# Kernel tuning notes

Hardware: AMD Instinct MI355X
Metric: run time of the kernel (lower is better)

The kernel has to match this reference:

```python
import jax, jax.numpy as jnp
import numpy as np

NUM_HEADS = 8
NEG_MASK = -1000.0  # original code masks with -1000, not -inf


def setup_inputs() -> dict:
    key = jax.random.key(0)
    ks = jax.random.split(key, 12)
    B, S, D = 4, 2048, 512
    HID, OUT = 512, 512
    dh = D // NUM_HEADS      # 64, per-head input dim
    eh = HID // NUM_HEADS    # 64, per-head hidden dim
    w = 0.02
    return {
        "q": jax.random.normal(ks[0], (B, S, D), dtype=jnp.float32),
        "k": jax.random.normal(ks[1], (B, S, D), dtype=jnp.float32),
        "v": jax.random.normal(ks[2], (B, S, D), dtype=jnp.float32),
        # Linear weights stored as [in, out] (transpose of torch convention)
        "Wq": jax.random.normal(ks[3], (dh, eh), dtype=jnp.float32) * w,
        "bq": jax.random.normal(ks[4], (eh,), dtype=jnp.float32) * w,
        "Wk": jax.random.normal(ks[5], (dh, eh), dtype=jnp.float32) * w,
        "bk": jax.random.normal(ks[6], (eh,), dtype=jnp.float32) * w,
        "Wv": jax.random.normal(ks[7], (dh, eh), dtype=jnp.float32) * w,
        "bv": jax.random.normal(ks[8], (eh,), dtype=jnp.float32) * w,
        "Wo": jax.random.normal(ks[9], (HID, OUT), dtype=jnp.float32) * w,
        "bo": jax.random.normal(ks[10], (OUT,), dtype=jnp.float32) * w,
        "valid_lens": jnp.maximum(jax.random.randint(ks[11], (B,), 0, S), 1),
        "max_len": S,
    }


def reference(q, k, v, Wq, bq, Wk, bk, Wv, bv, Wo, bo, valid_lens, max_len):
    B, S, D = q.shape
    H = NUM_HEADS
    # split into heads: [B, S, H, dh]; note the SAME projection weights are
    # shared across heads (as in the original module)
    qh = q.reshape(B, S, H, D // H)
    kh = k.reshape(B, S, H, D // H)
    vh = v.reshape(B, S, H, D // H)
    qp = jnp.einsum('bshd,de->bshe', qh, Wq) + bq  # [B,S,H,eh]
    kp = jnp.einsum('bshd,de->bshe', kh, Wk) + bk
    vp = jnp.einsum('bshd,de->bshe', vh, Wv) + bv
    scale = 1.0 / jnp.sqrt(jnp.asarray(qp.shape[-1], qp.dtype))
    scores = jnp.einsum('bshe,bthe->bhst', qp, kp) * scale  # [B,H,S,S]
    # key-padding mask: positions j >= valid_len get -1000 (original semantics)
    key_mask = jnp.arange(S)[None, :] < valid_lens[:, None]  # [B,S]
    scores = jnp.where(key_mask[:, None, None, :], scores, NEG_MASK)
    attn = jax.nn.softmax(scores, axis=-1)
    ctx = jnp.einsum('bhst,bthe->bshe', attn, vp).reshape(B, S, -1)  # head-major concat
    return jnp.einsum('bse,eo->bso', ctx, Wo) + bo
```

## Files before the change

### kernel.cpp

```cpp
#include <hip/hip_runtime.h>

#define S_LEN 2048
#define D_MODEL 512

typedef __attribute__((ext_vector_type(8))) short s8v;
typedef __attribute__((ext_vector_type(4))) float f4v;
typedef __attribute__((ext_vector_type(4))) short s4v;
typedef __attribute__((ext_vector_type(4))) int   i4v;
typedef __attribute__((ext_vector_type(2))) int   i2v;

#define MFMA __builtin_amdgcn_mfma_f32_16x16x32_bf16

__device__ inline short f2bf(float x) {
    union { float f; unsigned u; } v; v.f = x;
    unsigned r = v.u + 0x7fffu + ((v.u >> 16) & 1u);
    return (short)(r >> 16);
}
__device__ inline unsigned pack_bf2_trunc(float a, float b) {
    unsigned ua = __builtin_bit_cast(unsigned, a);
    unsigned ub = __builtin_bit_cast(unsigned, b);
    return (ua >> 16) | (ub & 0xffff0000u);
}

template <int C>
__device__ inline float dppf(float x) {
    int i = __builtin_bit_cast(int, x);
    i = __builtin_amdgcn_update_dpp(0, i, C, 0xF, 0xF, true);
    return __builtin_bit_cast(float, i);
}
__device__ inline float rowsum16(float x) {
    x += dppf<0xB1>(x);
    x += dppf<0x4E>(x);
    x += dppf<0x141>(x);
    x += dppf<0x140>(x);
    return x;
}

typedef const __attribute__((address_space(1))) void* gptr_t;
typedef __attribute__((address_space(3))) void* sptr_t;
__device__ inline void gload16(const void* g, void* s) {
    __builtin_amdgcn_global_load_lds((gptr_t)g, (sptr_t)s, 16, 0, 0);
}

__global__ __launch_bounds__(256) void prep_kernel(
    const float* __restrict__ Wo, short* __restrict__ WoT)
{
    __shared__ short t[64 * 65];
    const int bi = (blockIdx.x >> 3) * 64;
    const int bj = (blockIdx.x & 7) * 64;
    const int c = threadIdx.x & 63, rr = threadIdx.x >> 6;
#pragma unroll
    for (int r = 0; r < 16; r++) {
        int i = r * 4 + rr;
        t[c * 65 + i] = f2bf(Wo[(size_t)(bi + i) * 512 + bj + c]);
    }
    __syncthreads();
#pragma unroll
    for (int r = 0; r < 16; r++) {
        int o = r * 4 + rr;
        WoT[(size_t)(bj + o) * 512 + bi + c] = t[o * 65 + c];
    }
}

__global__ __launch_bounds__(256) void proj_kernel(
    const float* __restrict__ q, const float* __restrict__ k, const float* __restrict__ v,
    const float* __restrict__ Wq, const float* __restrict__ Wk, const float* __restrict__ Wv,
    const float* __restrict__ bq, const float* __restrict__ bk, const float* __restrict__ bv,
    short* __restrict__ qp, short* __restrict__ kfrag, short* __restrict__ vfrag)
{
    __shared__ short sm[128 * 64];

    const int t = blockIdx.z >> 2;
    const int b = blockIdx.z & 3;
    const int h = blockIdx.y;
    const int qt = blockIdx.x;
    const int w = threadIdx.x >> 6, lane = threadIdx.x & 63;
    const int l = lane & 15, qd = lane >> 4;

    const float* X    = (t == 0) ? q  : (t == 1) ? k  : v;
    const float* Wp   = (t == 0) ? Wq : (t == 1) ? Wk : Wv;
    const float* bias = (t == 0) ? bq : (t == 1) ? bk : bv;

    {
        const int d = threadIdx.x >> 2, c4 = threadIdx.x & 3;
        const float* src = Wp + d * 64 + c4 * 16;
        f4v x0 = *(const f4v*)(src);
        f4v x1 = *(const f4v*)(src + 4);
        f4v x2 = *(const f4v*)(src + 8);
        f4v x3 = *(const f4v*)(src + 12);
        float xs[16] = {x0[0],x0[1],x0[2],x0[3], x1[0],x1[1],x1[2],x1[3],
                        x2[0],x2[1],x2[2],x2[3], x3[0],x3[1],x3[2],x3[3]};
#pragma unroll
        for (int j = 0; j < 16; j++) {
            int e = c4 * 16 + j;
            int sidx = (e * 64 + d) ^ (((e >> 2) & 7) << 3);
            sm[sidx] = f2bf(xs[j]);
        }
    }
    __syncthreads();

    const int s0 = qt * 128 + w * 32;

    s8v a[2][2];
#pragma unroll
    for (int mt = 0; mt < 2; mt++)
#pragma unroll
        for (int kk = 0; kk < 2; kk++) {
            const float* p = X + (size_t)(b * S_LEN + s0 + mt * 16 + l) * 512 + h * 64 + kk * 32 + qd * 8;
            f4v x0 = *(const f4v*)p;
            f4v x1 = *(const f4v*)(p + 4);
            s8v fr;
            fr[0] = f2bf(x0[0]); fr[1] = f2bf(x0[1]); fr[2] = f2bf(x0[2]); fr[3] = f2bf(x0[3]);
            fr[4] = f2bf(x1[0]); fr[5] = f2bf(x1[1]); fr[6] = f2bf(x1[2]); fr[7] = f2bf(x1[3]);
            a[mt][kk] = fr;
        }
    s8v wf[4][2];
#pragma unroll
    for (int nt = 0; nt < 4; nt++) {
        int wrow = (t < 2) ? (4 * l + nt) : (nt * 16 + l);
        int key = ((wrow >> 2) & 7) << 3;
#pragma unroll
        for (int kk = 0; kk < 2; kk++)
            wf[nt][kk] = *(const s8v*)(sm + ((wrow * 64 + kk * 32 + qd * 8) ^ key));
    }

    const f4v fz = {0.f, 0.f, 0.f, 0.f};
    f4v acc[2][4];
#pragma unroll
    for (int mt = 0; mt < 2; mt++)
#pragma unroll
        for (int nt = 0; nt < 4; nt++) acc[mt][nt] = fz;

#pragma unroll
    for (int kk = 0; kk < 2; kk++)
#pragma unroll
        for (int nt = 0; nt < 4; nt++)
#pragma unroll
            for (int mt = 0; mt < 2; mt++)
                acc[mt][nt] = MFMA(a[mt][kk], wf[nt][kk], acc[mt][nt], 0, 0, 0);

    const float SC = 0.125f * 1.442695041f;

    if (t == 0) {
        float bbs[4];
#pragma unroll
        for (int nt = 0; nt < 4; nt++) bbs[nt] = bias[4 * l + nt];
#pragma unroll
        for (int mt = 0; mt < 2; mt++)
#pragma unroll
            for (int r = 0; r < 4; r++) {
                int s = s0 + mt * 16 + qd * 4 + r;
                s4v pk;
#pragma unroll
                for (int nt = 0; nt < 4; nt++)
                    pk[nt] = f2bf((acc[mt][nt][r] + bbs[nt]) * SC);
                *(s4v*)(qp + ((size_t)(b * 8 + h) * S_LEN + s) * 64 + 4 * l) = pk;
            }
        return;
    }

    __syncthreads();

    if (t == 1) {
        float bbs[4];
#pragma unroll
        for (int nt = 0; nt < 4; nt++) bbs[nt] = bias[4 * l + nt];
#pragma unroll
        for (int mt = 0; mt < 2; mt++)
#pragma unroll
            for (int r = 0; r < 4; r++) {
                int sl = w * 32 + mt * 16 + qd * 4 + r;
                s4v pk;
#pragma unroll
                for (int nt = 0; nt < 4; nt++) pk[nt] = f2bf(acc[mt][nt][r] + bbs[nt]);
                int sidx = (sl * 64 + 4 * l) ^ (((sl >> 2) & 7) << 3);
                *(s4v*)(sm + sidx) = pk;
            }
    } else {
#pragma unroll
        for (int nt = 0; nt < 4; nt++) {
            float bb = bias[nt * 16 + l];
            int e = nt * 16 + l;
            int key = ((e >> 2) & 7) << 3;
#pragma unroll
            for (int mt = 0; mt < 2; mt++) {
                s4v pk;
#pragma unroll
                for (int r = 0; r < 4; r++) pk[r] = f2bf(acc[mt][nt][r] + bb);
                int sidx = (e * 128 + w * 32 + mt * 16 + qd * 4) ^ key;
                *(s4v*)(sm + sidx) = pk;
            }
        }
    }
    __syncthreads();

    short* dst = (t == 1) ? kfrag : vfrag;
    const size_t obase0 = ((size_t)(b * 8 + h) * 32 + qt * 2) * 4096;
    const int f = threadIdx.x & 63, cp = threadIdx.x >> 6;
    const int fl = f & 15, fq = f >> 4;
#pragma unroll
    for (int tt = 0; tt < 2; tt++)
#pragma unroll
        for (int ci = 0; ci < 2; ci++) {
            int c = cp + ci * 4;
            int n2 = c >> 1, kk = c & 1;
            int sidx;
            if (t == 1) {
                int sl = tt * 64 + 4 * fl + n2;
                sidx = (sl * 64 + kk * 32 + fq * 8) ^ (((sl >> 2) & 7) << 3);
            } else {
                int e = 4 * fl + n2;
                sidx = (e * 128 + tt * 64 + kk * 32 + fq * 8) ^ (((e >> 2) & 7) << 3);
            }
            s8v x = *(const s8v*)(sm + sidx);
            *(s8v*)(dst + obase0 + tt * 4096 + c * 512 + f * 8) = x;
        }
}

__global__ __launch_bounds__(256, 2) void attn_kernel(
    const short* __restrict__ qp, const short* __restrict__ kfrag,
    const short* __restrict__ vfrag,
    const int* __restrict__ valid_lens, short* __restrict__ ctx)
{
    __shared__ alignas(16) short kbuf[2][8192];
    __shared__ alignas(16) short lP[4][32 * 72];

    const int gid = blockIdx.x;
    const int h  = gid & 7;
    int b        = (gid >> 3) & 3;
    const int qt = gid >> 5;
    b ^= 3 * ((gid >> 8) & 1);
    const int w = threadIdx.x >> 6, lane = threadIdx.x & 63;
    const int l = lane & 15, qd = lane >> 4;
    const int vlen = valid_lens[b];
    const int nt2 = (vlen + 127) >> 7;

    const int bh = b * 8 + h;
    const short* Qs = qp + (size_t)bh * S_LEN * 64;
    const short* Kf = kfrag + (size_t)bh * 32 * 4096;
    const short* Vf = vfrag + (size_t)bh * 32 * 4096;

    const int s0 = qt * 128 + w * 32;
    s8v qf[2][2];
#pragma unroll
    for (int mt = 0; mt < 2; mt++)
#pragma unroll
        for (int kk = 0; kk < 2; kk++)
            qf[mt][kk] = *(const s8v*)(Qs + (size_t)(s0 + mt * 16 + l) * 64 + kk * 32 + qd * 8);

    const f4v fz = {0.f, 0.f, 0.f, 0.f};
    f4v O[2][4];
    float lsum[2][4];
#pragma unroll
    for (int mt = 0; mt < 2; mt++)
#pragma unroll
        for (int r = 0; r < 4; r++) lsum[mt][r] = 0.f;
#pragma unroll
    for (int mt = 0; mt < 2; mt++)
#pragma unroll
        for (int ne = 0; ne < 4; ne++) O[mt][ne] = fz;

    short* lPw = lP[w];
    const int toff = threadIdx.x * 8;

#pragma unroll
    for (int r = 0; r < 4; r++)
        gload16(Kf + r * 2048 + toff, &kbuf[0][r * 2048 + toff]);
    __syncthreads();

    for (int j = 0; j < nt2; j++) {
        const int cur = j & 1;
        if (j + 1 < nt2) {
            const short* Ks = Kf + (size_t)(j + 1) * 8192;
#pragma unroll
            for (int r = 0; r < 4; r++)
                gload16(Ks + r * 2048 + toff, &kbuf[cur ^ 1][r * 2048 + toff]);
        }

#pragma unroll
        for (int st = 0; st < 2; st++) {
            const int kb = 2 * j + st;

            const short* Vb = Vf + (size_t)kb * 4096 + lane * 8;
            s8v vf[4][2];
#pragma unroll
            for (int ne = 0; ne < 4; ne++)
#pragma unroll
                for (int kk = 0; kk < 2; kk++)
                    vf[ne][kk] = *(const s8v*)(Vb + (ne * 2 + kk) * 512);

            const short* Kb = &kbuf[cur][st * 4096 + lane * 8];
            s8v kf[4][2];
#pragma unroll
            for (int nt = 0; nt < 4; nt++)
#pragma unroll
                for (int kk = 0; kk < 2; kk++)
                    kf[nt][kk] = *(const s8v*)(Kb + (nt * 2 + kk) * 512);

            f4v sf[2][4];
#pragma unroll
            for (int mt = 0; mt < 2; mt++)
#pragma unroll
                for (int nt = 0; nt < 4; nt++) sf[mt][nt] = fz;
            __builtin_amdgcn_s_setprio(1);
#pragma unroll
            for (int nt = 0; nt < 4; nt++)
#pragma unroll
                for (int mt = 0; mt < 2; mt++) {
                    sf[mt][nt] = MFMA(qf[mt][0], kf[nt][0], sf[mt][nt], 0, 0, 0);
                    sf[mt][nt] = MFMA(qf[mt][1], kf[nt][1], sf[mt][nt], 0, 0, 0);
                }
            __builtin_amdgcn_s_setprio(0);

            if (j == nt2 - 1) {
                int rem = vlen - kb * 64;
                if (rem < 64) {
#pragma unroll
                    for (int nt = 0; nt < 4; nt++)
                        if (4 * l + nt >= rem) {
#pragma unroll
                            for (int mt = 0; mt < 2; mt++)
#pragma unroll
                                for (int r = 0; r < 4; r++) sf[mt][nt][r] = -1e30f;
                        }
                }
            }

#pragma unroll
            for (int mt = 0; mt < 2; mt++)
#pragma unroll
                for (int r = 0; r < 4; r++) {
                    float p0 = __builtin_amdgcn_exp2f(sf[mt][0][r]);
                    float p1 = __builtin_amdgcn_exp2f(sf[mt][1][r]);
                    float p2 = __builtin_amdgcn_exp2f(sf[mt][2][r]);
                    float p3 = __builtin_amdgcn_exp2f(sf[mt][3][r]);
                    lsum[mt][r] += (p0 + p1) + (p2 + p3);
                    i2v pk;
                    pk[0] = (int)pack_bf2_trunc(p0, p1);
                    pk[1] = (int)pack_bf2_trunc(p2, p3);
                    *(i2v*)(lPw + (mt * 16 + qd * 4 + r) * 72 + 4 * l) = pk;
                }

            s8v pa[2][2];
#pragma unroll
            for (int mt = 0; mt < 2; mt++)
#pragma unroll
                for (int kk = 0; kk < 2; kk++)
                    pa[mt][kk] = *(const s8v*)(lPw + (mt * 16 + l) * 72 + kk * 32 + qd * 8);
            __builtin_amdgcn_s_setprio(1);
#pragma unroll
            for (int ne = 0; ne < 4; ne++)
#pragma unroll
                for (int mt = 0; mt < 2; mt++) {
                    O[mt][ne] = MFMA(pa[mt][0], vf[ne][0], O[mt][ne], 0, 0, 0);
                    O[mt][ne] = MFMA(pa[mt][1], vf[ne][1], O[mt][ne], 0, 0, 0);
                }
            __builtin_amdgcn_s_setprio(0);
        }

        __syncthreads();
    }

#pragma unroll
    for (int mt = 0; mt < 2; mt++)
#pragma unroll
        for (int r = 0; r < 4; r++) {
            float inv = 1.0f / rowsum16(lsum[mt][r]);
            int s = s0 + mt * 16 + qd * 4 + r;
            s4v pk;
#pragma unroll
            for (int ne = 0; ne < 4; ne++) pk[ne] = f2bf(O[mt][ne][r] * inv);
            *(s4v*)(ctx + ((size_t)(b * S_LEN + s)) * 512 + h * 64 + 4 * l) = pk;
        }
}

__global__ __launch_bounds__(256) void outproj_kernel(
    const short* __restrict__ ctx, const short* __restrict__ WoT,
    const float* __restrict__ bo, float* __restrict__ out)
{
    __shared__ short lB[64 * 520];

    const int rb = blockIdx.x * 128;
    const int nb = blockIdx.y * 64;
    const int w = threadIdx.x >> 6, lane = threadIdx.x & 63;
    const int l = lane & 15, qd = lane >> 4;

    {
        int n = threadIdx.x >> 2, c0 = threadIdx.x & 3;
#pragma unroll
        for (int i = 0; i < 16; i++) {
            int g = i * 4 + c0;
            i4v x = *(const i4v*)(WoT + (size_t)(nb + n) * 512 + g * 8);
            *(i4v*)(lB + n * 520 + g * 8) = x;
        }
    }
    __syncthreads();

    const f4v fz = {0.f, 0.f, 0.f, 0.f};
    f4v acc[2][4];
#pragma unroll
    for (int mt = 0; mt < 2; mt++)
#pragma unroll
        for (int nt = 0; nt < 4; nt++) acc[mt][nt] = fz;

    const short* actx0 = ctx + (size_t)(rb + w * 32 + l) * 512 + qd * 8;
    const short* actx1 = actx0 + (size_t)16 * 512;

    s8v afA[2], afB[2];
    afA[0] = *(const s8v*)(actx0);
    afA[1] = *(const s8v*)(actx1);

#pragma unroll
    for (int ko = 0; ko < 16; ko += 2) {
        afB[0] = *(const s8v*)(actx0 + (ko + 1) * 32);
        afB[1] = *(const s8v*)(actx1 + (ko + 1) * 32);
#pragma unroll
        for (int nt = 0; nt < 4; nt++) {
            s8v bfr = *(const s8v*)(lB + (nt * 16 + l) * 520 + ko * 32 + qd * 8);
#pragma unroll
            for (int mt = 0; mt < 2; mt++)
                acc[mt][nt] = MFMA(afA[mt], bfr, acc[mt][nt], 0, 0, 0);
        }
        if (ko + 2 < 16) {
            afA[0] = *(const s8v*)(actx0 + (ko + 2) * 32);
            afA[1] = *(const s8v*)(actx1 + (ko + 2) * 32);
        }
#pragma unroll
        for (int nt = 0; nt < 4; nt++) {
            s8v bfr = *(const s8v*)(lB + (nt * 16 + l) * 520 + (ko + 1) * 32 + qd * 8);
#pragma unroll
            for (int mt = 0; mt < 2; mt++)
                acc[mt][nt] = MFMA(afB[mt], bfr, acc[mt][nt], 0, 0, 0);
        }
    }

#pragma unroll
    for (int nt = 0; nt < 4; nt++) {
        float bias = bo[nb + nt * 16 + l];
#pragma unroll
        for (int mt = 0; mt < 2; mt++)
#pragma unroll
            for (int r = 0; r < 4; r++) {
                int row = rb + w * 32 + mt * 16 + qd * 4 + r;
                out[(size_t)row * 512 + nb + nt * 16 + l] = acc[mt][nt][r] + bias;
            }
    }
}

extern "C" void kernel_launch(void* const* d_in, const int* in_sizes, int n_in,
                              void* d_out, int out_size, void* d_ws, size_t ws_size,
                              hipStream_t stream)
{
    const float* q  = (const float*)d_in[0];
    const float* k  = (const float*)d_in[1];
    const float* v  = (const float*)d_in[2];
    const float* Wq = (const float*)d_in[3];
    const float* bq = (const float*)d_in[4];
    const float* Wk = (const float*)d_in[5];
    const float* bk = (const float*)d_in[6];
    const float* Wv = (const float*)d_in[7];
    const float* bv = (const float*)d_in[8];
    const float* Wo = (const float*)d_in[9];
    const float* bo = (const float*)d_in[10];
    const int*   vl = (const int*)d_in[11];
    float* out = (float*)d_out;

    char* ws = (char*)d_ws;
    const size_t SL = (size_t)4 * 8 * S_LEN * 64 * sizeof(short);
    short* qp    = (short*)(ws);
    short* ctx   = (short*)(ws + SL);
    short* kfrag = (short*)(ws + 2 * SL);
    short* vfrag = (short*)(ws + 3 * SL);
    short* WoT   = (short*)(ws + 4 * SL);

    prep_kernel<<<64, 256, 0, stream>>>(Wo, WoT);
    proj_kernel<<<dim3(16, 8, 12), 256, 0, stream>>>(q, k, v, Wq, Wk, Wv,
                                                     bq, bk, bv, qp, kfrag, vfrag);
    attn_kernel<<<512, 256, 0, stream>>>(qp, kfrag, vfrag, vl, ctx);
    outproj_kernel<<<dim3(64, 8), 256, 0, stream>>>(ctx, WoT, bo, out);
}
```

Baseline: 166.2 us.

## Fuse Q projection into attention kernel prologue

Moves the Q projection out of the separate projection kernel and into the start of the attention kernel. Each attention block now loads its fp32 query rows, projects them with MFMA against Wq staged in shared memory, and passes the scaled bf16 result through shared memory into registers. This removes the qp intermediate write and read-back in global memory and one third of the projection grid. In exchange it adds extra syncs and prologue latency in the attention kernel, and reuses kbuf and lP shared buffers as scratch.

```diff
diff --git a/kernel.cpp b/kernel.cpp
--- a/kernel.cpp
+++ b/kernel.cpp
@@ -63,23 +63,23 @@
 }
 
 __global__ __launch_bounds__(256) void proj_kernel(
-    const float* __restrict__ q, const float* __restrict__ k, const float* __restrict__ v,
-    const float* __restrict__ Wq, const float* __restrict__ Wk, const float* __restrict__ Wv,
-    const float* __restrict__ bq, const float* __restrict__ bk, const float* __restrict__ bv,
-    short* __restrict__ qp, short* __restrict__ kfrag, short* __restrict__ vfrag)
+    const float* __restrict__ k, const float* __restrict__ v,
+    const float* __restrict__ Wk, const float* __restrict__ Wv,
+    const float* __restrict__ bk, const float* __restrict__ bv,
+    short* __restrict__ kfrag, short* __restrict__ vfrag)
 {
     __shared__ short sm[128 * 64];
 
-    const int t = blockIdx.z >> 2;
+    const int t2 = blockIdx.z >> 2;
     const int b = blockIdx.z & 3;
     const int h = blockIdx.y;
     const int qt = blockIdx.x;
     const int w = threadIdx.x >> 6, lane = threadIdx.x & 63;
     const int l = lane & 15, qd = lane >> 4;
 
-    const float* X    = (t == 0) ? q  : (t == 1) ? k  : v;
-    const float* Wp   = (t == 0) ? Wq : (t == 1) ? Wk : Wv;
-    const float* bias = (t == 0) ? bq : (t == 1) ? bk : bv;
+    const float* X    = (t2 == 0) ? k  : v;
+    const float* Wp   = (t2 == 0) ? Wk : Wv;
+    const float* bias = (t2 == 0) ? bk : bv;
 
     {
         const int d = threadIdx.x >> 2, c4 = threadIdx.x & 3;
@@ -117,7 +117,7 @@
     s8v wf[4][2];
 #pragma unroll
     for (int nt = 0; nt < 4; nt++) {
-        int wrow = (t < 2) ? (4 * l + nt) : (nt * 16 + l);
+        int wrow = (t2 == 0) ? (4 * l + nt) : (nt * 16 + l);
         int key = ((wrow >> 2) & 7) << 3;
 #pragma unroll
         for (int kk = 0; kk < 2; kk++)
@@ -139,29 +139,9 @@
             for (int mt = 0; mt < 2; mt++)
                 acc[mt][nt] = MFMA(a[mt][kk], wf[nt][kk], acc[mt][nt], 0, 0, 0);
 
-    const float SC = 0.125f * 1.442695041f;
-
-    if (t == 0) {
-        float bbs[4];
-#pragma unroll
-        for (int nt = 0; nt < 4; nt++) bbs[nt] = bias[4 * l + nt];
-#pragma unroll
-        for (int mt = 0; mt < 2; mt++)
-#pragma unroll
-            for (int r = 0; r < 4; r++) {
-                int s = s0 + mt * 16 + qd * 4 + r;
-                s4v pk;
-#pragma unroll
-                for (int nt = 0; nt < 4; nt++)
-                    pk[nt] = f2bf((acc[mt][nt][r] + bbs[nt]) * SC);
-                *(s4v*)(qp + ((size_t)(b * 8 + h) * S_LEN + s) * 64 + 4 * l) = pk;
-            }
-        return;
-    }
-
-    __syncthreads();
-
-    if (t == 1) {
+    __syncthreads();
+
+    if (t2 == 0) {
         float bbs[4];
 #pragma unroll
         for (int nt = 0; nt < 4; nt++) bbs[nt] = bias[4 * l + nt];
@@ -194,7 +174,7 @@
     }
     __syncthreads();
 
-    short* dst = (t == 1) ? kfrag : vfrag;
+    short* dst = (t2 == 0) ? kfrag : vfrag;
     const size_t obase0 = ((size_t)(b * 8 + h) * 32 + qt * 2) * 4096;
     const int f = threadIdx.x & 63, cp = threadIdx.x >> 6;
     const int fl = f & 15, fq = f >> 4;
@@ -205,7 +185,7 @@
             int c = cp + ci * 4;
             int n2 = c >> 1, kk = c & 1;
             int sidx;
-            if (t == 1) {
+            if (t2 == 0) {
                 int sl = tt * 64 + 4 * fl + n2;
                 sidx = (sl * 64 + kk * 32 + fq * 8) ^ (((sl >> 2) & 7) << 3);
             } else {
@@ -218,8 +198,8 @@
 }
 
 __global__ __launch_bounds__(256, 2) void attn_kernel(
-    const short* __restrict__ qp, const short* __restrict__ kfrag,
-    const short* __restrict__ vfrag,
+    const float* __restrict__ q, const float* __restrict__ Wq, const float* __restrict__ bq,
+    const short* __restrict__ kfrag, const short* __restrict__ vfrag,
     const int* __restrict__ valid_lens, short* __restrict__ ctx)
 {
     __shared__ alignas(16) short kbuf[2][8192];
@@ -236,19 +216,105 @@
     const int nt2 = (vlen + 127) >> 7;
 
     const int bh = b * 8 + h;
-    const short* Qs = qp + (size_t)bh * S_LEN * 64;
     const short* Kf = kfrag + (size_t)bh * 32 * 4096;
     const short* Vf = vfrag + (size_t)bh * 32 * 4096;
 
     const int s0 = qt * 128 + w * 32;
+    const f4v fz = {0.f, 0.f, 0.f, 0.f};
+    const float SC = 0.125f * 1.442695041f;
+
+    short* lPw = lP[w];
+    const int toff = threadIdx.x * 8;
+
+#pragma unroll
+    for (int r = 0; r < 4; r++)
+        gload16(Kf + r * 2048 + toff, &kbuf[0][r * 2048 + toff]);
+
+    short* wsm = &kbuf[1][0];
+    short* qsm = &lP[0][0];
+    {
+        const int d = threadIdx.x >> 2, c4 = threadIdx.x & 3;
+        const float* src = Wq + d * 64 + c4 * 16;
+        f4v x0 = *(const f4v*)(src);
+        f4v x1 = *(const f4v*)(src + 4);
+        f4v x2 = *(const f4v*)(src + 8);
+        f4v x3 = *(const f4v*)(src + 12);
+        float xs[16] = {x0[0],x0[1],x0[2],x0[3], x1[0],x1[1],x1[2],x1[3],
+                        x2[0],x2[1],x2[2],x2[3], x3[0],x3[1],x3[2],x3[3]};
+#pragma unroll
+        for (int j = 0; j < 16; j++) {
+            int e = c4 * 16 + j;
+            int sidx = (e * 64 + d) ^ (((e >> 2) & 7) << 3);
+            wsm[sidx] = f2bf(xs[j]);
+        }
+    }
+    __syncthreads();
+
+    {
+        s8v a[2][2];
+#pragma unroll
+        for (int mt = 0; mt < 2; mt++)
+#pragma unroll
+            for (int kk = 0; kk < 2; kk++) {
+                const float* p = q + (size_t)(b * S_LEN + s0 + mt * 16 + l) * 512 + h * 64 + kk * 32 + qd * 8;
+                f4v x0 = *(const f4v*)p;
+                f4v x1 = *(const f4v*)(p + 4);
+                s8v fr;
+                fr[0] = f2bf(x0[0]); fr[1] = f2bf(x0[1]); fr[2] = f2bf(x0[2]); fr[3] = f2bf(x0[3]);
+                fr[4] = f2bf(x1[0]); fr[5] = f2bf(x1[1]); fr[6] = f2bf(x1[2]); fr[7] = f2bf(x1[3]);
+                a[mt][kk] = fr;
+            }
+        s8v wf2[4][2];
+#pragma unroll
+        for (int nt = 0; nt < 4; nt++) {
+            int wrow = 4 * l + nt;
+            int key = ((wrow >> 2) & 7) << 3;
+#pragma unroll
+            for (int kk = 0; kk < 2; kk++)
+                wf2[nt][kk] = *(const s8v*)(wsm + ((wrow * 64 + kk * 32 + qd * 8) ^ key));
+        }
+        f4v qacc[2][4];
+#pragma unroll
+        for (int mt = 0; mt < 2; mt++)
+#pragma unroll
+            for (int nt = 0; nt < 4; nt++) qacc[mt][nt] = fz;
+#pragma unroll
+        for (int kk = 0; kk < 2; kk++)
+#pragma unroll
+            for (int nt = 0; nt < 4; nt++)
+#pragma unroll
+                for (int mt = 0; mt < 2; mt++)
+                    qacc[mt][nt] = MFMA(a[mt][kk], wf2[nt][kk], qacc[mt][nt], 0, 0, 0);
+
+        float bbs[4];
+#pragma unroll
+        for (int nt = 0; nt < 4; nt++) bbs[nt] = bq[4 * l + nt];
+#pragma unroll
+        for (int mt = 0; mt < 2; mt++)
+#pragma unroll
+            for (int r = 0; r < 4; r++) {
+                int sl = w * 32 + mt * 16 + qd * 4 + r;
+                s4v pk;
+#pragma unroll
+                for (int nt = 0; nt < 4; nt++)
+                    pk[nt] = f2bf((qacc[mt][nt][r] + bbs[nt]) * SC);
+                int sidx = (sl * 64 + 4 * l) ^ (((sl >> 2) & 7) << 3);
+                *(s4v*)(qsm + sidx) = pk;
+            }
+    }
+    __syncthreads();
+
     s8v qf[2][2];
 #pragma unroll
-    for (int mt = 0; mt < 2; mt++)
+    for (int mt = 0; mt < 2; mt++) {
+        int sl = w * 32 + mt * 16 + l;
+        int key = ((sl >> 2) & 7) << 3;
 #pragma unroll
         for (int kk = 0; kk < 2; kk++)
-            qf[mt][kk] = *(const s8v*)(Qs + (size_t)(s0 + mt * 16 + l) * 64 + kk * 32 + qd * 8);
-
-    const f4v fz = {0.f, 0.f, 0.f, 0.f};
+            qf[mt][kk] = *(const s8v*)(qsm + ((sl * 64 + kk * 32 + qd * 8) ^ key));
+    }
+    __syncthreads();
+
     f4v O[2][4];
     float lsum[2][4];
 #pragma unroll
@@ -259,14 +325,6 @@
     for (int mt = 0; mt < 2; mt++)
 #pragma unroll
         for (int ne = 0; ne < 4; ne++) O[mt][ne] = fz;
-
-    short* lPw = lP[w];
-    const int toff = threadIdx.x * 8;
-
-#pragma unroll
-    for (int r = 0; r < 4; r++)
-        gload16(Kf + r * 2048 + toff, &kbuf[0][r * 2048 + toff]);
-    __syncthreads();
 
     for (int j = 0; j < nt2; j++) {
         const int cur = j & 1;
@@ -467,15 +525,13 @@
 
     char* ws = (char*)d_ws;
     const size_t SL = (size_t)4 * 8 * S_LEN * 64 * sizeof(short);
-    short* qp    = (short*)(ws);
-    short* ctx   = (short*)(ws + SL);
-    short* kfrag = (short*)(ws + 2 * SL);
-    short* vfrag = (short*)(ws + 3 * SL);
-    short* WoT   = (short*)(ws + 4 * SL);
+    short* ctx   = (short*)(ws);
+    short* kfrag = (short*)(ws + SL);
+    short* vfrag = (short*)(ws + 2 * SL);
+    short* WoT   = (short*)(ws + 3 * SL);
 
     prep_kernel<<<64, 256, 0, stream>>>(Wo, WoT);
-    proj_kernel<<<dim3(16, 8, 12), 256, 0, stream>>>(q, k, v, Wq, Wk, Wv,
-                                                     bq, bk, bv, qp, kfrag, vfrag);
-    attn_kernel<<<512, 256, 0, stream>>>(qp, kfrag, vfrag, vl, ctx);
+    proj_kernel<<<dim3(16, 8, 8), 256, 0, stream>>>(k, v, Wk, Wv, bk, bv, kfrag, vfrag);
+    attn_kernel<<<512, 256, 0, stream>>>(q, Wq, bq, kfrag, vfrag, vl, ctx);
     outproj_kernel<<<dim3(64, 8), 256, 0, stream>>>(ctx, WoT, bo, out);
 }
```

Result: no change. 166.1 us (-0.1%).
